# Optimization experiments

Measured on AMD Instinct MI355X. Metric: run time of the kernel, lower is better.

## Reference

```python
import jax, jax.numpy as jnp
import numpy as np

B, N, C, H, W = 2, 8, 128, 120, 360
LN_EPS = 1e-5  # torch F.layer_norm default
SM_EPS = 1e-8  # masked_softmax epsilon


def layer_norm(x):
    m = x.mean(-1, keepdims=True)
    v = ((x - m) ** 2).mean(-1, keepdims=True)
    return (x - m) / jnp.sqrt(v + LN_EPS)


def setup_inputs() -> dict:
    key = jax.random.key(0)
    ks = jax.random.split(key, 8)
    feat = jax.random.normal(ks[0], (B, N, C, H, W), jnp.float32)
    init_prob = jax.random.randint(ks[1], (B,), 0, N, jnp.int32)  # initial camera index per sample
    keep_cams = jnp.ones((B, N), dtype=bool)
    cam_emb = jax.random.normal(ks[2], (N, N), jnp.float32) * 0.02
    s = 1.0 / np.sqrt(C).astype(np.float32)
    W1 = jax.random.normal(ks[3], (C, C), jnp.float32) * s
    b1 = jnp.zeros((C,), jnp.float32)
    W2 = jax.random.normal(ks[4], (C, C), jnp.float32) * s
    b2 = jnp.zeros((C,), jnp.float32)
    Wp = jax.random.normal(ks[5], (N, C), jnp.float32) * 0.02  # cam_pred weight (no bias)
    return dict(feat=feat, init_prob=init_prob, keep_cams=keep_cams,
                cam_emb=cam_emb, W1=W1, b1=b1, W2=W2, b2=b2, Wp=Wp)


def reference(feat, init_prob, keep_cams, cam_emb, W1, b1, W2, b2, Wp):
    # Eval path of CamPredModule (not training -> hard=True, masked_softmax, argmax one-hot).
    Bc, Nc = feat.shape[:2]
    ip = jax.nn.one_hot(init_prob, Nc, dtype=jnp.int32) > 0        # [B,N] bool one-hot init camera
    ipf = ip.astype(feat.dtype)
    # aggregate_init, aggregation='max': mask then max over cameras
    init_feat = (feat * ipf[:, :, None, None, None]).max(1)        # [B,C,H,W]
    # router
    ce = layer_norm(ipf @ cam_emb)                                 # [B,N]
    cf = init_feat.max((2, 3))                                     # [B,C] spatial amax
    h = jax.nn.relu(cf @ W1.T + b1)
    h = jax.nn.relu(h @ W2.T + b2)
    cp = layer_norm(h @ Wp.T) / 10.0                               # [B,N]
    logits = cp + ce
    cand = (~ip) & keep_cams                                       # cam_candidate mask
    masked_exp = jnp.exp(logits) * cand.astype(logits.dtype)
    select_prob = masked_exp / (masked_exp.sum(1, keepdims=True) + SM_EPS)
    select_hard = jax.nn.one_hot(jnp.argmax(select_prob, axis=1), Nc, dtype=feat.dtype)  # [B,N]
    # aggregate_init_selection, aggregation='max'
    select_feat = jnp.einsum('bnchw,bn->bchw', feat, select_hard)  # [B,C,H,W]
    overall_feat = jnp.maximum(init_feat, select_feat)
    return overall_feat, ce, cp, select_hard
```

## Files before the change

### kernel.cpp

```cpp
#include <hip/hip_runtime.h>
#include <float.h>
#include <math.h>

#define B_   2
#define N_   8
#define C_   128
#define H_   120
#define W_   360
#define HW_  (H_ * W_)
#define CHW_ (C_ * HW_)
#define SEG_ 4

#define WS_PARTIAL_FLOATS (B_ * C_ * SEG_)

__global__ void k_spatial_max(const float* __restrict__ feat,
                              const int* __restrict__ init_prob,
                              float* __restrict__ partial) {
    const int row = blockIdx.x;
    const int seg = blockIdx.y;
    const int b = row >> 7;
    const int c = row & (C_ - 1);
    const int cam = init_prob[b];

    const float4* src = (const float4*)(feat + (size_t)b * N_ * CHW_
                                             + (size_t)cam * CHW_
                                             + (size_t)c * HW_);
    const int nvec = HW_ / 4;
    const int per  = nvec / SEG_;
    const int start = seg * per;

    float m = -FLT_MAX;
    for (int i = start + threadIdx.x; i < start + per; i += blockDim.x) {
        float4 v = src[i];
        m = fmaxf(m, fmaxf(fmaxf(v.x, v.y), fmaxf(v.z, v.w)));
    }
    for (int off = 32; off > 0; off >>= 1)
        m = fmaxf(m, __shfl_down(m, off));

    __shared__ float s[4];
    const int lane = threadIdx.x & 63;
    const int wv   = threadIdx.x >> 6;
    if (lane == 0) s[wv] = m;
    __syncthreads();
    if (threadIdx.x == 0) {
        float r = fmaxf(fmaxf(s[0], s[1]), fmaxf(s[2], s[3]));
        partial[row * SEG_ + seg] = r;
    }
}

__global__ void k_router(const float* __restrict__ partial,
                         const int* __restrict__ init_prob,
                         const float* __restrict__ cam_emb,
                         const float* __restrict__ W1, const float* __restrict__ b1,
                         const float* __restrict__ W2, const float* __restrict__ b2,
                         const float* __restrict__ Wp,
                         float* __restrict__ out_ce,
                         float* __restrict__ out_cp,
                         float* __restrict__ out_sh,
                         int* __restrict__ sel_ws) {
    __shared__ float cf[B_][C_];
    __shared__ float h1[B_][C_];
    __shared__ float h2[B_][C_];
    __shared__ float g[B_][N_];

    const int t = threadIdx.x;
    const int b = t >> 7;
    const int i = t & (C_ - 1);

    float m = -FLT_MAX;
    #pragma unroll
    for (int s2 = 0; s2 < SEG_; ++s2)
        m = fmaxf(m, partial[t * SEG_ + s2]);
    cf[b][i] = fmaxf(m, 0.f);
    __syncthreads();

    float acc = b1[i];
    for (int j = 0; j < C_; ++j)
        acc += W1[i * C_ + j] * cf[b][j];
    h1[b][i] = fmaxf(acc, 0.f);
    __syncthreads();

    acc = b2[i];
    for (int j = 0; j < C_; ++j)
        acc += W2[i * C_ + j] * h1[b][j];
    h2[b][i] = fmaxf(acc, 0.f);
    __syncthreads();

    if (t < B_ * N_) {
        const int bb = t >> 3;
        const int n  = t & (N_ - 1);
        float a = 0.f;
        for (int j = 0; j < C_; ++j)
            a += Wp[n * C_ + j] * h2[bb][j];
        g[bb][n] = a;
    }
    __syncthreads();

    if (t < B_) {
        const int bb = t;
        const int cam = init_prob[bb];

        float x[N_], ce[N_], cp[N_];
        float mean = 0.f;
        #pragma unroll
        for (int n = 0; n < N_; ++n) { x[n] = cam_emb[cam * N_ + n]; mean += x[n]; }
        mean *= (1.f / N_);
        float var = 0.f;
        #pragma unroll
        for (int n = 0; n < N_; ++n) { float d = x[n] - mean; var += d * d; }
        var *= (1.f / N_);
        float inv = 1.f / sqrtf(var + 1e-5f);
        #pragma unroll
        for (int n = 0; n < N_; ++n) ce[n] = (x[n] - mean) * inv;

        mean = 0.f;
        #pragma unroll
        for (int n = 0; n < N_; ++n) mean += g[bb][n];
        mean *= (1.f / N_);
        var = 0.f;
        #pragma unroll
        for (int n = 0; n < N_; ++n) { float d = g[bb][n] - mean; var += d * d; }
        var *= (1.f / N_);
        inv = 1.f / sqrtf(var + 1e-5f);
        #pragma unroll
        for (int n = 0; n < N_; ++n) cp[n] = (g[bb][n] - mean) * inv * 0.1f;

        float me[N_];
        float sum = 0.f;
        #pragma unroll
        for (int n = 0; n < N_; ++n) {
            float lg = cp[n] + ce[n];
            float e = (n == cam) ? 0.f : expf(lg);
            me[n] = e;
            sum += e;
        }
        const float denom = sum + 1e-8f;
        float best = -1.f;
        int bestn = 0;
        #pragma unroll
        for (int n = 0; n < N_; ++n) {
            float p = me[n] / denom;
            if (p > best) { best = p; bestn = n; }
        }

        #pragma unroll
        for (int n = 0; n < N_; ++n) {
            out_ce[bb * N_ + n] = ce[n];
            out_cp[bb * N_ + n] = cp[n];
            out_sh[bb * N_ + n] = (n == bestn) ? 1.f : 0.f;
        }
        sel_ws[bb] = bestn;
    }
}

__global__ void k_combine(const float* __restrict__ feat,
                          const int* __restrict__ init_prob,
                          const int* __restrict__ sel_ws,
                          float* __restrict__ out) {
    const int b = blockIdx.y;
    const int cam0 = init_prob[b];
    const int cam1 = sel_ws[b];

    const float4* a = (const float4*)(feat + (size_t)b * N_ * CHW_ + (size_t)cam0 * CHW_);
    const float4* s = (const float4*)(feat + (size_t)b * N_ * CHW_ + (size_t)cam1 * CHW_);
    float4* o = (float4*)(out + (size_t)b * CHW_);

    const int nvec = CHW_ / 4;
    for (int i = blockIdx.x * blockDim.x + threadIdx.x; i < nvec;
         i += gridDim.x * blockDim.x) {
        float4 va = a[i];
        float4 vs = s[i];
        float4 r;
        r.x = fmaxf(fmaxf(va.x, 0.f), vs.x);
        r.y = fmaxf(fmaxf(va.y, 0.f), vs.y);
        r.z = fmaxf(fmaxf(va.z, 0.f), vs.z);
        r.w = fmaxf(fmaxf(va.w, 0.f), vs.w);
        o[i] = r;
    }
}

extern "C" void kernel_launch(void* const* d_in, const int* in_sizes, int n_in,
                              void* d_out, int out_size, void* d_ws, size_t ws_size,
                              hipStream_t stream) {
    const float* feat      = (const float*)d_in[0];
    const int*   init_prob = (const int*)d_in[1];
    const float* cam_emb   = (const float*)d_in[3];
    const float* W1        = (const float*)d_in[4];
    const float* b1        = (const float*)d_in[5];
    const float* W2        = (const float*)d_in[6];
    const float* b2        = (const float*)d_in[7];
    const float* Wp        = (const float*)d_in[8];

    float* out = (float*)d_out;
    float* out_overall = out;
    float* out_ce      = out + (size_t)B_ * CHW_;
    float* out_cp      = out_ce + B_ * N_;
    float* out_sh      = out_cp + B_ * N_;

    float* ws_partial = (float*)d_ws;
    int*   ws_sel     = (int*)((float*)d_ws + WS_PARTIAL_FLOATS);

    k_spatial_max<<<dim3(B_ * C_, SEG_), 256, 0, stream>>>(feat, init_prob, ws_partial);

    k_router<<<1, 256, 0, stream>>>(ws_partial, init_prob, cam_emb,
                                    W1, b1, W2, b2, Wp,
                                    out_ce, out_cp, out_sh, ws_sel);

    k_combine<<<dim3(2048, B_), 256, 0, stream>>>(feat, init_prob, ws_sel, out_overall);
}
```

Baseline: 44.59 us.

## Fuse router into spatial-max kernel via last-block counter and unroll combine loads

The spatial-max and router kernels are merged. Each block atomically increments a counter, and the last block to finish runs the MLP/softmax router using partial maxima read through atomic loads. This removes a separate launch and its dependency gap, at the cost of an extra memset to reset the counter. The combine kernel now uses an exact grid with four float4 loads per thread issued up front to increase memory-level parallelism. The router matvecs are also vectorized with float4.

Measured after the change: 69.48 us. 1.56x slower.

```diff
diff --git a/kernel.cpp b/kernel.cpp
--- a/kernel.cpp
+++ b/kernel.cpp
@@ -10,100 +10,122 @@
 #define HW_  (H_ * W_)
 #define CHW_ (C_ * HW_)
 #define SEG_ 4
-
-#define WS_PARTIAL_FLOATS (B_ * C_ * SEG_)
-
-__global__ void k_spatial_max(const float* __restrict__ feat,
-                              const int* __restrict__ init_prob,
-                              float* __restrict__ partial) {
+#define NPART_ (B_ * C_ * SEG_)
+
+__global__ void k_max_router(const float* __restrict__ feat,
+                             const int* __restrict__ init_prob,
+                             const float* __restrict__ cam_emb,
+                             const float* __restrict__ W1, const float* __restrict__ b1,
+                             const float* __restrict__ W2, const float* __restrict__ b2,
+                             const float* __restrict__ Wp,
+                             float* __restrict__ out_ce,
+                             float* __restrict__ out_cp,
+                             float* __restrict__ out_sh,
+                             float* __restrict__ partial,
+                             int* __restrict__ counter,
+                             int* __restrict__ sel_ws) {
     const int row = blockIdx.x;
     const int seg = blockIdx.y;
     const int b = row >> 7;
     const int c = row & (C_ - 1);
     const int cam = init_prob[b];
 
-    const float4* src = (const float4*)(feat + (size_t)b * N_ * CHW_
-                                             + (size_t)cam * CHW_
+    const float4* src = (const float4*)(feat + (size_t)(b * N_ + cam) * CHW_
                                              + (size_t)c * HW_);
-    const int nvec = HW_ / 4;
-    const int per  = nvec / SEG_;
+    const int per   = (HW_ / 4) / SEG_;
     const int start = seg * per;
 
     float m = -FLT_MAX;
-    for (int i = start + threadIdx.x; i < start + per; i += blockDim.x) {
+    for (int i = start + threadIdx.x; i < start + per; i += 256) {
         float4 v = src[i];
-        m = fmaxf(m, fmaxf(fmaxf(v.x, v.y), fmaxf(v.z, v.w)));
+        m = fmaxf(fmaxf(v.x, v.y), fmaxf(fmaxf(v.z, v.w), m));
     }
     for (int off = 32; off > 0; off >>= 1)
         m = fmaxf(m, __shfl_down(m, off));
 
-    __shared__ float s[4];
-    const int lane = threadIdx.x & 63;
-    const int wv   = threadIdx.x >> 6;
-    if (lane == 0) s[wv] = m;
+    __shared__ float sred[4];
+    __shared__ int lastFlag;
+    if ((threadIdx.x & 63) == 0) sred[threadIdx.x >> 6] = m;
     __syncthreads();
     if (threadIdx.x == 0) {
-        float r = fmaxf(fmaxf(s[0], s[1]), fmaxf(s[2], s[3]));
-        partial[row * SEG_ + seg] = r;
-    }
-}
-
-__global__ void k_router(const float* __restrict__ partial,
-                         const int* __restrict__ init_prob,
-                         const float* __restrict__ cam_emb,
-                         const float* __restrict__ W1, const float* __restrict__ b1,
-                         const float* __restrict__ W2, const float* __restrict__ b2,
-                         const float* __restrict__ Wp,
-                         float* __restrict__ out_ce,
-                         float* __restrict__ out_cp,
-                         float* __restrict__ out_sh,
-                         int* __restrict__ sel_ws) {
-    __shared__ float cf[B_][C_];
-    __shared__ float h1[B_][C_];
-    __shared__ float h2[B_][C_];
+        float r = fmaxf(fmaxf(sred[0], sred[1]), fmaxf(sred[2], sred[3]));
+        __hip_atomic_store(&partial[row * SEG_ + seg], r,
+                           __ATOMIC_RELAXED, __HIP_MEMORY_SCOPE_AGENT);
+        int old = __hip_atomic_fetch_add(counter, 1,
+                                         __ATOMIC_ACQ_REL, __HIP_MEMORY_SCOPE_AGENT);
+        lastFlag = (old == NPART_ - 1);
+    }
+    __syncthreads();
+    if (!lastFlag) return;
+
+    __shared__ __align__(16) float cf[B_][C_];
+    __shared__ __align__(16) float h1[B_][C_];
+    __shared__ __align__(16) float h2[B_][C_];
     __shared__ float g[B_][N_];
 
-    const int t = threadIdx.x;
-    const int b = t >> 7;
-    const int i = t & (C_ - 1);
-
-    float m = -FLT_MAX;
-    #pragma unroll
-    for (int s2 = 0; s2 < SEG_; ++s2)
-        m = fmaxf(m, partial[t * SEG_ + s2]);
-    cf[b][i] = fmaxf(m, 0.f);
-    __syncthreads();
-
-    float acc = b1[i];
-    for (int j = 0; j < C_; ++j)
-        acc += W1[i * C_ + j] * cf[b][j];
-    h1[b][i] = fmaxf(acc, 0.f);
-    __syncthreads();
-
-    acc = b2[i];
-    for (int j = 0; j < C_; ++j)
-        acc += W2[i * C_ + j] * h1[b][j];
-    h2[b][i] = fmaxf(acc, 0.f);
+    const int t  = threadIdx.x;
+    const int bb = t >> 7;
+    const int i  = t & (C_ - 1);
+
+    float mm = -FLT_MAX;
+    #pragma unroll
+    for (int s2 = 0; s2 < SEG_; ++s2) {
+        float v = __hip_atomic_load(&partial[t * SEG_ + s2],
+                                    __ATOMIC_RELAXED, __HIP_MEMORY_SCOPE_AGENT);
+        mm = fmaxf(mm, v);
+    }
+    cf[bb][i] = fmaxf(mm, 0.f);
+    __syncthreads();
+
+    {
+        float acc = b1[i];
+        const float4* wr = (const float4*)(W1 + i * C_);
+        const float4* xv = (const float4*)cf[bb];
+        #pragma unroll 8
+        for (int j = 0; j < C_ / 4; ++j) {
+            float4 w = wr[j], x = xv[j];
+            acc += w.x * x.x + w.y * x.y + w.z * x.z + w.w * x.w;
+        }
+        h1[bb][i] = fmaxf(acc, 0.f);
+    }
+    __syncthreads();
+
+    {
+        float acc = b2[i];
+        const float4* wr = (const float4*)(W2 + i * C_);
+        const float4* xv = (const float4*)h1[bb];
+        #pragma unroll 8
+        for (int j = 0; j < C_ / 4; ++j) {
+            float4 w = wr[j], x = xv[j];
+            acc += w.x * x.x + w.y * x.y + w.z * x.z + w.w * x.w;
+        }
+        h2[bb][i] = fmaxf(acc, 0.f);
+    }
     __syncthreads();
 
     if (t < B_ * N_) {
-        const int bb = t >> 3;
+        const int gb = t >> 3;
         const int n  = t & (N_ - 1);
         float a = 0.f;
-        for (int j = 0; j < C_; ++j)
-            a += Wp[n * C_ + j] * h2[bb][j];
-        g[bb][n] = a;
+        const float4* wr = (const float4*)(Wp + n * C_);
+        const float4* xv = (const float4*)h2[gb];
+        #pragma unroll 8
+        for (int j = 0; j < C_ / 4; ++j) {
+            float4 w = wr[j], x = xv[j];
+            a += w.x * x.x + w.y * x.y + w.z * x.z + w.w * x.w;
+        }
+        g[gb][n] = a;
     }
     __syncthreads();
 
     if (t < B_) {
-        const int bb = t;
-        const int cam = init_prob[bb];
+        const int pb  = t;
+        const int pc  = init_prob[pb];
 
         float x[N_], ce[N_], cp[N_];
         float mean = 0.f;
         #pragma unroll
-        for (int n = 0; n < N_; ++n) { x[n] = cam_emb[cam * N_ + n]; mean += x[n]; }
+        for (int n = 0; n < N_; ++n) { x[n] = cam_emb[pc * N_ + n]; mean += x[n]; }
         mean *= (1.f / N_);
         float var = 0.f;
         #pragma unroll
@@ -115,22 +137,21 @@
 
         mean = 0.f;
         #pragma unroll
-        for (int n = 0; n < N_; ++n) mean += g[bb][n];
+        for (int n = 0; n < N_; ++n) mean += g[pb][n];
         mean *= (1.f / N_);
         var = 0.f;
         #pragma unroll
-        for (int n = 0; n < N_; ++n) { float d = g[bb][n] - mean; var += d * d; }
+        for (int n = 0; n < N_; ++n) { float d = g[pb][n] - mean; var += d * d; }
         var *= (1.f / N_);
         inv = 1.f / sqrtf(var + 1e-5f);
         #pragma unroll
-        for (int n = 0; n < N_; ++n) cp[n] = (g[bb][n] - mean) * inv * 0.1f;
+        for (int n = 0; n < N_; ++n) cp[n] = (g[pb][n] - mean) * inv * 0.1f;
 
         float me[N_];
         float sum = 0.f;
         #pragma unroll
         for (int n = 0; n < N_; ++n) {
-            float lg = cp[n] + ce[n];
-            float e = (n == cam) ? 0.f : expf(lg);
+            float e = (n == pc) ? 0.f : expf(cp[n] + ce[n]);
             me[n] = e;
             sum += e;
         }
@@ -145,11 +166,11 @@
 
         #pragma unroll
         for (int n = 0; n < N_; ++n) {
-            out_ce[bb * N_ + n] = ce[n];
-            out_cp[bb * N_ + n] = cp[n];
-            out_sh[bb * N_ + n] = (n == bestn) ? 1.f : 0.f;
-        }
-        sel_ws[bb] = bestn;
+            out_ce[pb * N_ + n] = ce[n];
+            out_cp[pb * N_ + n] = cp[n];
+            out_sh[pb * N_ + n] = (n == bestn) ? 1.f : 0.f;
+        }
+        sel_ws[pb] = bestn;
     }
 }
 
@@ -161,21 +182,25 @@
     const int cam0 = init_prob[b];
     const int cam1 = sel_ws[b];
 
-    const float4* a = (const float4*)(feat + (size_t)b * N_ * CHW_ + (size_t)cam0 * CHW_);
-    const float4* s = (const float4*)(feat + (size_t)b * N_ * CHW_ + (size_t)cam1 * CHW_);
+    const float4* a = (const float4*)(feat + (size_t)(b * N_ + cam0) * CHW_);
+    const float4* s = (const float4*)(feat + (size_t)(b * N_ + cam1) * CHW_);
     float4* o = (float4*)(out + (size_t)b * CHW_);
 
-    const int nvec = CHW_ / 4;
-    for (int i = blockIdx.x * blockDim.x + threadIdx.x; i < nvec;
-         i += gridDim.x * blockDim.x) {
-        float4 va = a[i];
-        float4 vs = s[i];
+    const int base = blockIdx.x * 1024 + threadIdx.x;
+
+    float4 va[4], vs[4];
+    #pragma unroll
+    for (int k = 0; k < 4; ++k) va[k] = a[base + k * 256];
+    #pragma unroll
+    for (int k = 0; k < 4; ++k) vs[k] = s[base + k * 256];
+    #pragma unroll
+    for (int k = 0; k < 4; ++k) {
         float4 r;
-        r.x = fmaxf(fmaxf(va.x, 0.f), vs.x);
-        r.y = fmaxf(fmaxf(va.y, 0.f), vs.y);
-        r.z = fmaxf(fmaxf(va.z, 0.f), vs.z);
-        r.w = fmaxf(fmaxf(va.w, 0.f), vs.w);
-        o[i] = r;
+        r.x = fmaxf(fmaxf(va[k].x, 0.f), vs[k].x);
+        r.y = fmaxf(fmaxf(va[k].y, 0.f), vs[k].y);
+        r.z = fmaxf(fmaxf(va[k].z, 0.f), vs[k].z);
+        r.w = fmaxf(fmaxf(va[k].w, 0.f), vs[k].w);
+        o[base + k * 256] = r;
     }
 }
 
@@ -198,13 +223,14 @@
     float* out_sh      = out_cp + B_ * N_;
 
     float* ws_partial = (float*)d_ws;
-    int*   ws_sel     = (int*)((float*)d_ws + WS_PARTIAL_FLOATS);
-
-    k_spatial_max<<<dim3(B_ * C_, SEG_), 256, 0, stream>>>(feat, init_prob, ws_partial);
-
-    k_router<<<1, 256, 0, stream>>>(ws_partial, init_prob, cam_emb,
-                                    W1, b1, W2, b2, Wp,
-                                    out_ce, out_cp, out_sh, ws_sel);
-
-    k_combine<<<dim3(2048, B_), 256, 0, stream>>>(feat, init_prob, ws_sel, out_overall);
+    int*   ws_sel     = (int*)(ws_partial + NPART_);
+    int*   ws_counter = ws_sel + B_;
+
+    hipMemsetAsync(ws_counter, 0, sizeof(int), stream);
+
+    k_max_router<<<dim3(B_ * C_, SEG_), 256, 0, stream>>>(
+        feat, init_prob, cam_emb, W1, b1, W2, b2, Wp,
+        out_ce, out_cp, out_sh, ws_partial, ws_counter, ws_sel);
+
+    k_combine<<<dim3(1350, B_), 256, 0, stream>>>(feat, init_prob, ws_sel, out_overall);
 }
```
